# Optimization experiments

Measured on AMD Instinct MI355X. Metric: run time of the kernel, lower is better.

The kernel has to match this reference:

```python
import jax, jax.numpy as jnp
import numpy as np

ALPHA = 1.5
BETA = 0.5
AVG_RATIO = 1.0
SUM_TIMESTEPS = 28000
RANK = 8
K_TOP = RANK * RANK  # k = weight_1_a.shape[1] * weight_2_a.shape[1]


def setup_inputs() -> dict:
    key = jax.random.key(0)
    ks = jax.random.split(key, 5)
    B, S, D_IN, D_OUT = 2, 4096, 4096, 4096
    return {
        "hidden_states": jax.random.normal(ks[0], (B, S, D_IN), dtype=jnp.float32),
        "weight_1_a": jax.random.normal(ks[1], (D_OUT, RANK), dtype=jnp.float32) * 0.02,
        "weight_1_b": jax.random.normal(ks[2], (RANK, D_IN), dtype=jnp.float32) * 0.02,
        "weight_2_a": jax.random.normal(ks[3], (D_OUT, RANK), dtype=jnp.float32) * 0.02,
        "weight_2_b": jax.random.normal(ks[4], (RANK, D_IN), dtype=jnp.float32) * 0.02,
        "timestep": 1,
    }


def reference(hidden_states, weight_1_a, weight_1_b, weight_2_a, weight_2_b, timestep):
    # Low-rank expansions: [out, rank] @ [rank, in] -> [out, in]
    matrix1 = weight_1_a @ weight_1_b
    matrix2 = weight_2_a @ weight_2_b
    top_k_sum1 = jax.lax.top_k(jnp.abs(matrix1).ravel(), K_TOP)[0].sum()
    top_k_sum2 = jax.lax.top_k(jnp.abs(matrix2).ravel(), K_TOP)[0].sum()
    time_ratio = timestep % SUM_TIMESTEPS
    scale = (ALPHA * time_ratio / SUM_TIMESTEPS + BETA) % ALPHA  # pattern 's*'
    temp_ratio = (top_k_sum1 / AVG_RATIO) / (top_k_sum2 * scale)
    weight = jnp.where(temp_ratio > 1.0, matrix1, matrix2)  # [out, in]
    # F.linear: x @ W^T
    return jnp.einsum("bsi,oi->bso", hidden_states, weight)
```

## Files before the change

kernel.cpp:

```cpp
#include <hip/hip_runtime.h>
#include <stdint.h>

#define D 4096
#define RANK 8
#define ALPHA 1.5f
#define BETA 0.5f
#define SUM_TIMESTEPS 28000
#define K_TOP 64
#define NBINS 1024

typedef float f32x4 __attribute__((ext_vector_type(4)));

#define WS_GCNT_OFF 256
#define WS_GSUM_OFF (256 + 2 * NBINS * 4)
#define WS_BMAX_OFF (WS_GSUM_OFF + 2 * NBINS * 8)
#define WS_T_OFF    (WS_BMAX_OFF + 2048)

#define FIX_NUM 2.74877906944e11f
#define FIX_INV 3.637978807091713e-12

__device__ __forceinline__ float dot4v(f32x4 a, f32x4 b) {
    return fmaf(a.x, b.x, fmaf(a.y, b.y, fmaf(a.z, b.z, a.w * b.w)));
}

__global__ __launch_bounds__(256) void k_pass_max(
    const float* __restrict__ wa1, const float* __restrict__ wb1,
    const float* __restrict__ wa2, const float* __restrict__ wb2,
    unsigned* __restrict__ gz, unsigned* __restrict__ bmax) {
    const int tid = threadIdx.x;
    const int mat = blockIdx.y;
    const int bid = blockIdx.x;
    if (mat == 0 && tid < 24) gz[bid * 24 + tid] = 0u;

    const float* __restrict__ wa = mat ? wa2 : wa1;
    const float* __restrict__ wb = mat ? wb2 : wb1;
    const int i0 = (bid & 3) * 1024 + tid * 4;
    const int obase = (bid >> 2) * 64;

    __shared__ float was[64][8];
    if (tid < 128)
        ((f32x4*)was)[tid] = ((const f32x4*)(wa + (size_t)obase * RANK))[tid];

    f32x4 wbv[RANK];
#pragma unroll
    for (int r = 0; r < RANK; ++r)
        wbv[r] = *(const f32x4*)(wb + r * D + i0);
    __syncthreads();

    float vmax = 0.f;
#pragma unroll 4
    for (int oo = 0; oo < 64; ++oo) {
        const f32x4 w03 = *(const f32x4*)&was[oo][0];
        const f32x4 w47 = *(const f32x4*)&was[oo][4];
        f32x4 s = {0.f, 0.f, 0.f, 0.f};
        const float a[8] = {w03.x, w03.y, w03.z, w03.w, w47.x, w47.y, w47.z, w47.w};
#pragma unroll
        for (int r = 0; r < RANK; ++r) {
            s.x = fmaf(a[r], wbv[r].x, s.x);
            s.y = fmaf(a[r], wbv[r].y, s.y);
            s.z = fmaf(a[r], wbv[r].z, s.z);
            s.w = fmaf(a[r], wbv[r].w, s.w);
        }
        vmax = fmaxf(vmax, fmaxf(fmaxf(fabsf(s.x), fabsf(s.y)),
                                 fmaxf(fabsf(s.z), fabsf(s.w))));
    }
    for (int off = 32; off; off >>= 1)
        vmax = fmaxf(vmax, __shfl_xor(vmax, off, 64));
    __shared__ float smax[4];
    const int wave = tid >> 6, lane = tid & 63;
    if (lane == 0) smax[wave] = vmax;
    __syncthreads();
    if (tid == 0) {
        float m = fmaxf(fmaxf(smax[0], smax[1]), fmaxf(smax[2], smax[3]));
        bmax[mat * 256 + bid] = __float_as_uint(m);
    }
}

__device__ __forceinline__ float block_max256(const unsigned* __restrict__ bmax,
                                              int mat, int tid, float* redm) {
    const int wave = tid >> 6, lane = tid & 63;
    float m = 0.f;
    if (tid < 256) m = __uint_as_float(bmax[mat * 256 + tid]);
    for (int off = 32; off; off >>= 1)
        m = fmaxf(m, __shfl_xor(m, off, 64));
    if (tid < 256 && lane == 0) redm[wave] = m;
    __syncthreads();
    return fmaxf(fmaxf(redm[0], redm[1]), fmaxf(redm[2], redm[3]));
}

__global__ __launch_bounds__(256) void k_pass_hist(
    const float* __restrict__ wa1, const float* __restrict__ wb1,
    const float* __restrict__ wa2, const float* __restrict__ wb2,
    const unsigned* __restrict__ bmax,
    unsigned* __restrict__ gcnt, unsigned long long* __restrict__ gsum) {
    __shared__ unsigned lcnt[NBINS];
    __shared__ unsigned long long lsum[NBINS];
    __shared__ float was[64][8];
    __shared__ float redm[4];
    const int tid = threadIdx.x;
    const int mat = blockIdx.y;
    for (int b = tid; b < NBINS; b += 256) { lcnt[b] = 0u; lsum[b] = 0ull; }

    const float* __restrict__ wa = mat ? wa2 : wa1;
    const float* __restrict__ wb = mat ? wb2 : wb1;
    const int i0 = (blockIdx.x & 3) * 1024 + tid * 4;
    const int obase = (blockIdx.x >> 2) * 64;
    if (tid < 128)
        ((f32x4*)was)[tid] = ((const f32x4*)(wa + (size_t)obase * RANK))[tid];

    const float M = block_max256(bmax, mat, tid, redm);
    const float T = 0.5f * M;
    const float fix = FIX_NUM / M;
    const unsigned bitsT = __float_as_uint(T);

    f32x4 wbv[RANK];
#pragma unroll
    for (int r = 0; r < RANK; ++r)
        wbv[r] = *(const f32x4*)(wb + r * D + i0);

#pragma unroll 2
    for (int oo = 0; oo < 64; ++oo) {
        const f32x4 w03 = *(const f32x4*)&was[oo][0];
        const f32x4 w47 = *(const f32x4*)&was[oo][4];
        f32x4 s = {0.f, 0.f, 0.f, 0.f};
        const float a[8] = {w03.x, w03.y, w03.z, w03.w, w47.x, w47.y, w47.z, w47.w};
#pragma unroll
        for (int r = 0; r < RANK; ++r) {
            s.x = fmaf(a[r], wbv[r].x, s.x);
            s.y = fmaf(a[r], wbv[r].y, s.y);
            s.z = fmaf(a[r], wbv[r].z, s.z);
            s.w = fmaf(a[r], wbv[r].w, s.w);
        }
        const float av[4] = {fabsf(s.x), fabsf(s.y), fabsf(s.z), fabsf(s.w)};
#pragma unroll
        for (int j = 0; j < 4; ++j) {
            if (av[j] >= T) {
                unsigned k = (__float_as_uint(av[j]) - bitsT) >> 13;
                if (k > NBINS - 1u) k = NBINS - 1u;
                atomicAdd(&lcnt[k], 1u);
                atomicAdd(&lsum[k], (unsigned long long)(av[j] * fix));
            }
        }
    }
    __syncthreads();
    unsigned* __restrict__ gc = gcnt + (size_t)mat * NBINS;
    unsigned long long* __restrict__ gs = gsum + (size_t)mat * NBINS;
    for (int b = tid; b < NBINS; b += 256) {
        unsigned c = lcnt[b];
        if (c) {
            atomicAdd(&gc[b], c);
            atomicAdd(&gs[b], lsum[b]);
        }
    }
}

__global__ __launch_bounds__(1024) void k_select(
    unsigned* __restrict__ hdr, const unsigned* __restrict__ bmax,
    const unsigned* __restrict__ gcnt, const unsigned long long* __restrict__ gsum,
    const int* __restrict__ tsp) {
    __shared__ unsigned sc[NBINS];
    __shared__ unsigned long long ss[NBINS];
    __shared__ float res[2];
    __shared__ float Ms[2];
    __shared__ float redm[4];
    __shared__ int sB;
    const int b = threadIdx.x;

    for (int mat = 0; mat < 2; ++mat) {
        float M = block_max256(bmax, mat, b, redm);
        if (b == 0) Ms[mat] = M;
        __syncthreads();
    }

    for (int mat = 0; mat < 2; ++mat) {
        if (b == 0) sB = -1;
        const unsigned c0 = gcnt[(size_t)mat * NBINS + b];
        const unsigned long long s0 = gsum[(size_t)mat * NBINS + b];
        __syncthreads();
        sc[b] = c0;
        ss[b] = s0;
        __syncthreads();
        for (int step = 1; step < NBINS; step <<= 1) {
            unsigned c2 = 0u; unsigned long long s2 = 0ull;
            if (b + step < NBINS) { c2 = sc[b + step]; s2 = ss[b + step]; }
            __syncthreads();
            sc[b] += c2;
            ss[b] += s2;
            __syncthreads();
        }
        if (sc[b] >= K_TOP && (b == NBINS - 1 || sc[b + 1] < K_TOP)) sB = b;
        __syncthreads();
        if (b == 0) {
            const double inv = (double)Ms[mat] * FIX_INV;
            float total;
            if (sB < 0) {
                total = (float)((double)ss[0] * inv);
            } else {
                const int B = sB;
                const unsigned cAbove = (B + 1 < NBINS) ? sc[B + 1] : 0u;
                const unsigned long long sAbove = (B + 1 < NBINS) ? ss[B + 1] : 0ull;
                const unsigned cb = sc[B] - cAbove;
                const unsigned long long sb = ss[B] - sAbove;
                const unsigned need = K_TOP - cAbove;
                total = (float)((double)sAbove * inv)
                      + (float)((double)sb * inv) * ((float)need / (float)cb);
            }
            res[mat] = total;
        }
        __syncthreads();
    }
    if (b == 0) {
        const int tr = (*tsp) % SUM_TIMESTEPS;
        const float scale = fmodf(ALPHA * (float)tr / (float)SUM_TIMESTEPS + BETA, ALPHA);
        const float temp_ratio = res[0] / (res[1] * scale);
        hdr[4] = (temp_ratio > 1.0f) ? 1u : 0u;
    }
}

__global__ __launch_bounds__(1024) void k_t(
    const float* __restrict__ h,
    const float* __restrict__ wb1, const float* __restrict__ wb2,
    const unsigned* __restrict__ hdr,
    float* __restrict__ t) {
    extern __shared__ float wbs[];
    const int tid = threadIdx.x;
    const int wave = tid >> 6, lane = tid & 63;
    const float* __restrict__ wb = hdr[4] ? wb1 : wb2;

    {
        const f32x4* __restrict__ src = (const f32x4*)wb;
        f32x4* __restrict__ dst = (f32x4*)wbs;
#pragma unroll
        for (int s = 0; s < 8; ++s)
            dst[s * 1024 + tid] = src[s * 1024 + tid];
    }
    __syncthreads();

    const size_t m0 = (size_t)blockIdx.x * 32 + wave * 2;

    float acc[2][RANK];
#pragma unroll
    for (int row = 0; row < 2; ++row)
#pragma unroll
        for (int r = 0; r < RANK; ++r) acc[row][r] = 0.f;

#pragma unroll 2
    for (int k = 0; k < 16; ++k) {
        const int i = k * 256 + lane * 4;
        const f32x4 h0 = *(const f32x4*)(h + m0 * D + i);
        const f32x4 h1 = *(const f32x4*)(h + (m0 + 1) * D + i);
        f32x4 wbv[RANK];
#pragma unroll
        for (int r = 0; r < RANK; ++r)
            wbv[r] = *(const f32x4*)&wbs[r * D + i];
#pragma unroll
        for (int r = 0; r < RANK; ++r) {
            acc[0][r] = fmaf(h0.x, wbv[r].x, fmaf(h0.y, wbv[r].y,
                        fmaf(h0.z, wbv[r].z, fmaf(h0.w, wbv[r].w, acc[0][r]))));
            acc[1][r] = fmaf(h1.x, wbv[r].x, fmaf(h1.y, wbv[r].y,
                        fmaf(h1.z, wbv[r].z, fmaf(h1.w, wbv[r].w, acc[1][r]))));
        }
    }

#pragma unroll
    for (int row = 0; row < 2; ++row)
#pragma unroll
        for (int r = 0; r < RANK; ++r)
#pragma unroll
            for (int off = 32; off; off >>= 1)
                acc[row][r] += __shfl_xor(acc[row][r], off, 64);
    if (lane == 0) {
        const f32x4 v0 = {acc[0][0], acc[0][1], acc[0][2], acc[0][3]};
        const f32x4 v1 = {acc[0][4], acc[0][5], acc[0][6], acc[0][7]};
        const f32x4 v2 = {acc[1][0], acc[1][1], acc[1][2], acc[1][3]};
        const f32x4 v3 = {acc[1][4], acc[1][5], acc[1][6], acc[1][7]};
        f32x4* __restrict__ dst = (f32x4*)(t + m0 * RANK);
        dst[0] = v0; dst[1] = v1; dst[2] = v2; dst[3] = v3;
    }
}

__global__ __launch_bounds__(256) void k_o(
    const float* __restrict__ t,
    const float* __restrict__ wa1, const float* __restrict__ wa2,
    const unsigned* __restrict__ hdr,
    float* __restrict__ out) {
    const int tid = threadIdx.x;
    const int wave = tid >> 6, lane = tid & 63;
    const float* __restrict__ wa = hdr[4] ? wa1 : wa2;
    const int cslice = blockIdx.x & 3;
    const size_t m0 = (size_t)(blockIdx.x >> 2) * 32;
    const int o0 = cslice * 1024 + wave * 256 + lane * 4;

    __shared__ float ts[32][8];
    if (tid < 64)
        ((f32x4*)ts)[tid] = *(const f32x4*)(t + m0 * RANK + tid * 4);

    f32x4 A[8];
#pragma unroll
    for (int j = 0; j < 8; ++j)
        A[j] = *(const f32x4*)(wa + (size_t)o0 * RANK + j * 4);
    __syncthreads();

#pragma unroll 4
    for (int row = 0; row < 32; ++row) {
        const f32x4 t03 = *(const f32x4*)&ts[row][0];
        const f32x4 t47 = *(const f32x4*)&ts[row][4];
        f32x4 ov;
        ov.x = dot4v(A[0], t03) + dot4v(A[1], t47);
        ov.y = dot4v(A[2], t03) + dot4v(A[3], t47);
        ov.z = dot4v(A[4], t03) + dot4v(A[5], t47);
        ov.w = dot4v(A[6], t03) + dot4v(A[7], t47);
        *(f32x4*)(out + (m0 + row) * D + o0) = ov;
    }
}

extern "C" void kernel_launch(void* const* d_in, const int* in_sizes, int n_in,
                              void* d_out, int out_size, void* d_ws, size_t ws_size,
                              hipStream_t stream) {
    const float* h   = (const float*)d_in[0];
    const float* wa1 = (const float*)d_in[1];
    const float* wb1 = (const float*)d_in[2];
    const float* wa2 = (const float*)d_in[3];
    const float* wb2 = (const float*)d_in[4];
    const int*   ts  = (const int*)d_in[5];
    float* out = (float*)d_out;

    const int rows = in_sizes[0] / D;

    unsigned* hdr  = (unsigned*)d_ws;
    unsigned* gcnt = (unsigned*)((char*)d_ws + WS_GCNT_OFF);
    unsigned long long* gsum = (unsigned long long*)((char*)d_ws + WS_GSUM_OFF);
    unsigned* bmax = (unsigned*)((char*)d_ws + WS_BMAX_OFF);
    float*    tbuf = (float*)((char*)d_ws + WS_T_OFF);

    (void)hipFuncSetAttribute((const void*)k_t,
                              hipFuncAttributeMaxDynamicSharedMemorySize,
                              RANK * D * (int)sizeof(float));

    hipLaunchKernelGGL(k_pass_max, dim3(256, 2), dim3(256), 0, stream,
                       wa1, wb1, wa2, wb2, gcnt, bmax);
    hipLaunchKernelGGL(k_pass_hist, dim3(256, 2), dim3(256), 0, stream,
                       wa1, wb1, wa2, wb2, bmax, gcnt, gsum);
    hipLaunchKernelGGL(k_select, dim3(1), dim3(1024), 0, stream,
                       hdr, bmax, gcnt, gsum, ts);
    hipLaunchKernelGGL(k_t, dim3(rows / 32), dim3(1024),
                       RANK * D * sizeof(float), stream,
                       h, wb1, wb2, hdr, tbuf);
    hipLaunchKernelGGL(k_o, dim3(4 * (rows / 32)), dim3(256), 0, stream,
                       tbuf, wa1, wa2, hdr, out);
}
```

Before: 107.7 us.

## Drop LDS staging of low-rank B in k_t; register double-buffer loads with 4 rows per wave

```diff
diff --git a/kernel.cpp b/kernel.cpp
--- a/kernel.cpp
+++ b/kernel.cpp
@@ -217,65 +217,73 @@
     }
 }
 
-__global__ __launch_bounds__(1024) void k_t(
+__device__ __forceinline__ void kt_load(const float* __restrict__ h,
+                                        const float* __restrict__ wb,
+                                        size_t m0, int i,
+                                        f32x4 hv[4], f32x4 wv[RANK]) {
+#pragma unroll
+    for (int row = 0; row < 4; ++row)
+        hv[row] = *(const f32x4*)(h + (m0 + row) * D + i);
+#pragma unroll
+    for (int r = 0; r < RANK; ++r)
+        wv[r] = *(const f32x4*)(wb + r * D + i);
+}
+
+__device__ __forceinline__ void kt_fma(const f32x4 hv[4], const f32x4 wv[RANK],
+                                       float acc[4][RANK]) {
+#pragma unroll
+    for (int row = 0; row < 4; ++row)
+#pragma unroll
+        for (int r = 0; r < RANK; ++r)
+            acc[row][r] = fmaf(hv[row].x, wv[r].x,
+                          fmaf(hv[row].y, wv[r].y,
+                          fmaf(hv[row].z, wv[r].z,
+                          fmaf(hv[row].w, wv[r].w, acc[row][r]))));
+}
+
+__global__ __launch_bounds__(256) void k_t(
     const float* __restrict__ h,
     const float* __restrict__ wb1, const float* __restrict__ wb2,
     const unsigned* __restrict__ hdr,
     float* __restrict__ t) {
-    extern __shared__ float wbs[];
     const int tid = threadIdx.x;
     const int wave = tid >> 6, lane = tid & 63;
     const float* __restrict__ wb = hdr[4] ? wb1 : wb2;
-
-    {
-        const f32x4* __restrict__ src = (const f32x4*)wb;
-        f32x4* __restrict__ dst = (f32x4*)wbs;
-#pragma unroll
-        for (int s = 0; s < 8; ++s)
-            dst[s * 1024 + tid] = src[s * 1024 + tid];
-    }
-    __syncthreads();
-
-    const size_t m0 = (size_t)blockIdx.x * 32 + wave * 2;
-
-    float acc[2][RANK];
-#pragma unroll
-    for (int row = 0; row < 2; ++row)
+    const size_t m0 = ((size_t)blockIdx.x * 4 + wave) * 4;
+    const int ib = lane * 4;
+
+    float acc[4][RANK];
+#pragma unroll
+    for (int row = 0; row < 4; ++row)
 #pragma unroll
         for (int r = 0; r < RANK; ++r) acc[row][r] = 0.f;
 
-#pragma unroll 2
-    for (int k = 0; k < 16; ++k) {
-        const int i = k * 256 + lane * 4;
-        const f32x4 h0 = *(const f32x4*)(h + m0 * D + i);
-        const f32x4 h1 = *(const f32x4*)(h + (m0 + 1) * D + i);
-        f32x4 wbv[RANK];
-#pragma unroll
-        for (int r = 0; r < RANK; ++r)
-            wbv[r] = *(const f32x4*)&wbs[r * D + i];
-#pragma unroll
-        for (int r = 0; r < RANK; ++r) {
-            acc[0][r] = fmaf(h0.x, wbv[r].x, fmaf(h0.y, wbv[r].y,
-                        fmaf(h0.z, wbv[r].z, fmaf(h0.w, wbv[r].w, acc[0][r]))));
-            acc[1][r] = fmaf(h1.x, wbv[r].x, fmaf(h1.y, wbv[r].y,
-                        fmaf(h1.z, wbv[r].z, fmaf(h1.w, wbv[r].w, acc[1][r]))));
-        }
-    }
-
-#pragma unroll
-    for (int row = 0; row < 2; ++row)
+    f32x4 hA[4], wA[RANK], hB[4], wB[RANK];
+    kt_load(h, wb, m0, ib, hA, wA);
+#pragma unroll
+    for (int k = 0; k < 16; k += 2) {
+        kt_load(h, wb, m0, (k + 1) * 256 + ib, hB, wB);
+        kt_fma(hA, wA, acc);
+        if (k < 14)
+            kt_load(h, wb, m0, (k + 2) * 256 + ib, hA, wA);
+        kt_fma(hB, wB, acc);
+    }
+
+#pragma unroll
+    for (int row = 0; row < 4; ++row)
 #pragma unroll
         for (int r = 0; r < RANK; ++r)
 #pragma unroll
             for (int off = 32; off; off >>= 1)
                 acc[row][r] += __shfl_xor(acc[row][r], off, 64);
     if (lane == 0) {
-        const f32x4 v0 = {acc[0][0], acc[0][1], acc[0][2], acc[0][3]};
-        const f32x4 v1 = {acc[0][4], acc[0][5], acc[0][6], acc[0][7]};
-        const f32x4 v2 = {acc[1][0], acc[1][1], acc[1][2], acc[1][3]};
-        const f32x4 v3 = {acc[1][4], acc[1][5], acc[1][6], acc[1][7]};
-        f32x4* __restrict__ dst = (f32x4*)(t + m0 * RANK);
-        dst[0] = v0; dst[1] = v1; dst[2] = v2; dst[3] = v3;
+#pragma unroll
+        for (int row = 0; row < 4; ++row) {
+            const f32x4 v0 = {acc[row][0], acc[row][1], acc[row][2], acc[row][3]};
+            const f32x4 v1 = {acc[row][4], acc[row][5], acc[row][6], acc[row][7]};
+            f32x4* __restrict__ dst = (f32x4*)(t + (m0 + row) * RANK);
+            dst[0] = v0; dst[1] = v1;
+        }
     }
 }
 
@@ -333,18 +341,13 @@
     unsigned* bmax = (unsigned*)((char*)d_ws + WS_BMAX_OFF);
     float*    tbuf = (float*)((char*)d_ws + WS_T_OFF);
 
-    (void)hipFuncSetAttribute((const void*)k_t,
-                              hipFuncAttributeMaxDynamicSharedMemorySize,
-                              RANK * D * (int)sizeof(float));
-
     hipLaunchKernelGGL(k_pass_max, dim3(256, 2), dim3(256), 0, stream,
                        wa1, wb1, wa2, wb2, gcnt, bmax);
     hipLaunchKernelGGL(k_pass_hist, dim3(256, 2), dim3(256), 0, stream,
                        wa1, wb1, wa2, wb2, bmax, gcnt, gsum);
     hipLaunchKernelGGL(k_select, dim3(1), dim3(1024), 0, stream,
                        hdr, bmax, gcnt, gsum, ts);
-    hipLaunchKernelGGL(k_t, dim3(rows / 32), dim3(1024),
-                       RANK * D * sizeof(float), stream,
+    hipLaunchKernelGGL(k_t, dim3(rows / 16), dim3(256), 0, stream,
                        h, wb1, wb2, hdr, tbuf);
     hipLaunchKernelGGL(k_o, dim3(4 * (rows / 32)), dim3(256), 0, stream,
                        tbuf, wa1, wa2, hdr, out);
```

New measurement: 97.88 us. 9.1% less time.
